# Performance work log

Hardware: AMD Instinct MI355X
Metric: run time of the kernel (lower is better)

Reference implementation:

```python
import jax, jax.numpy as jnp
import numpy as np

B, L, H, T = 32, 512, 1024, 67


def setup_inputs() -> dict:
    key = jax.random.key(0)
    ks = jax.random.split(key, 7)
    hidden = jax.random.normal(ks[0], (B, L, H), jnp.float32)
    labels = jax.random.randint(ks[1], (B, L), 0, T)
    # contiguous valid-length mask; torchcrf requires mask[:, 0] == True
    lengths = jax.random.randint(ks[2], (B,), L // 2, L + 1)
    mask = jnp.arange(L)[None, :] < lengths[:, None]  # bool [B, L]
    W = jax.random.normal(ks[3], (H, T), jnp.float32) / np.float32(np.sqrt(H))
    b = jnp.zeros((T,), jnp.float32)
    u = lambda k, s: jax.random.uniform(k, s, jnp.float32, -0.1, 0.1)  # torchcrf init
    return dict(hidden=hidden, W=W, b=b,
                start_transitions=u(ks[4], (T,)),
                end_transitions=u(ks[5], (T,)),
                transitions=u(ks[6], (T, T)),
                labels=labels, mask=mask)


def crf_log_likelihood(emissions, tags, mask, start, end, trans):
    # emissions [B,L,T], tags [B,L] int, mask [B,L] bool. Returns sum llh over batch.
    maskf = mask.astype(emissions.dtype)
    # --- numerator: score of gold path (fully vectorized) ---
    emit = jnp.take_along_axis(emissions, tags[..., None], axis=2)[..., 0]  # [B,L]
    tr = trans[tags[:, :-1], tags[:, 1:]]                                   # [B,L-1]
    seq_ends = mask.sum(1) - 1
    last_tags = jnp.take_along_axis(tags, seq_ends[:, None], axis=1)[:, 0]
    numerator = (start[tags[:, 0]] + (emit * maskf).sum(1)
                 + (tr * maskf[:, 1:]).sum(1) + end[last_tags])
    # --- denominator: log-partition via batched scan over time ---
    alpha0 = start[None, :] + emissions[:, 0]  # [B,T]
    def step(alpha, x):
        e_t, m_t = x  # [B,T], [B]
        nxt = jax.scipy.special.logsumexp(
            alpha[:, :, None] + trans[None, :, :] + e_t[:, None, :], axis=1)
        return jnp.where(m_t[:, None], nxt, alpha), None
    xs = (jnp.moveaxis(emissions[:, 1:], 1, 0), jnp.moveaxis(mask[:, 1:], 1, 0))
    alpha, _ = jax.lax.scan(step, alpha0, xs)
    denominator = jax.scipy.special.logsumexp(alpha + end[None, :], axis=1)
    return (numerator - denominator).sum()


def viterbi_decode(emissions, mask, start, end, trans):
    # Returns padded [B,L] int tags (padded positions set to 0).
    score0 = start[None, :] + emissions[:, 0]  # [B,T]
    def fstep(score, x):
        e_t, m_t = x
        bc = score[:, :, None] + trans[None, :, :]  # [B, prev T, cur T]
        idx = jnp.argmax(bc, axis=1)                # [B,T] best prev tag per cur
        best = jnp.max(bc, axis=1) + e_t
        return jnp.where(m_t[:, None], best, score), idx
    xs = (jnp.moveaxis(emissions[:, 1:], 1, 0), jnp.moveaxis(mask[:, 1:], 1, 0))
    score, hist = jax.lax.scan(fstep, score0, xs)   # hist [L-1,B,T]
    last = jnp.argmax(score + end[None, :], axis=1)  # [B] tag at last valid pos
    def bstep(cur, x):
        h_t, m_t = x
        out = cur  # tag at position t
        prev = jnp.take_along_axis(h_t, cur[:, None], axis=1)[:, 0]
        return jnp.where(m_t, prev, cur), out
    xs_rev = (hist[::-1], jnp.moveaxis(mask[:, 1:], 1, 0)[::-1])
    cur0, outs = jax.lax.scan(bstep, last, xs_rev)
    tags = jnp.concatenate([cur0[None, :], outs[::-1]], axis=0).T  # [B,L]
    return jnp.where(mask, tags, 0)


def reference(hidden, W, b, start_transitions, end_transitions, transitions, labels, mask):
    # dropout is identity in eval; leaky_relu negative_slope=0.01 matches torch default
    x = jax.nn.leaky_relu(hidden)
    token_scores = jax.nn.log_softmax(x @ W + b, axis=-1)  # [B,L,T]
    llh = crf_log_likelihood(token_scores, labels, mask,
                             start_transitions, end_transitions, transitions)
    loss = -llh / hidden.shape[0]
    tags = viterbi_decode(token_scores, mask,
                          start_transitions, end_transitions, transitions)
    return loss, tags
```

## Files before the change

kernel.cpp:

```cpp
#include <hip/hip_runtime.h>
#include <math.h>

constexpr int NB = 32;
constexpr int NL = 512;
constexpr int NH = 1024;
constexpr int NT = 67;

__device__ __forceinline__ float wave_max_f(float v) {
#pragma unroll
  for (int o = 32; o > 0; o >>= 1) v = fmaxf(v, __shfl_xor(v, o));
  return v;
}
__device__ __forceinline__ float wave_min_f(float v) {
#pragma unroll
  for (int o = 32; o > 0; o >>= 1) v = fminf(v, __shfl_xor(v, o));
  return v;
}
__device__ __forceinline__ float wave_sum_f(float v) {
#pragma unroll
  for (int o = 32; o > 0; o >>= 1) v += __shfl_xor(v, o);
  return v;
}
__device__ __forceinline__ int wave_sum_i(int v) {
#pragma unroll
  for (int o = 32; o > 0; o >>= 1) v += __shfl_xor(v, o);
  return v;
}

#define DPPF(OLDV, X, CTRL)                                                     \
  __int_as_float(__builtin_amdgcn_update_dpp(__float_as_int(OLDV),              \
                                             __float_as_int(X), (CTRL), 0xf,   \
                                             0xf, false))

__device__ __forceinline__ float wave_max_dpp(float x) {
  x = fmaxf(x, DPPF(x, x, 0x111));
  x = fmaxf(x, DPPF(x, x, 0x112));
  x = fmaxf(x, DPPF(x, x, 0x114));
  x = fmaxf(x, DPPF(x, x, 0x118));
  x = fmaxf(x, DPPF(x, x, 0x142));
  x = fmaxf(x, DPPF(x, x, 0x143));
  return __int_as_float(__builtin_amdgcn_readlane(__float_as_int(x), 63));
}
__device__ __forceinline__ float wave_sum_dpp(float x) {
  x += DPPF(0.f, x, 0x111);
  x += DPPF(0.f, x, 0x112);
  x += DPPF(0.f, x, 0x114);
  x += DPPF(0.f, x, 0x118);
  x += DPPF(0.f, x, 0x142);
  x += DPPF(0.f, x, 0x143);
  return __int_as_float(__builtin_amdgcn_readlane(__float_as_int(x), 63));
}

#define LGKM_BARRIER() asm volatile("s_waitcnt lgkmcnt(0)" ::: "memory")

__device__ __forceinline__ float rdlane(float v, int l) {
  return __int_as_float(__builtin_amdgcn_readlane(__float_as_int(v), l));
}
__device__ __forceinline__ float rdfirst(float v) {
  return __int_as_float(__builtin_amdgcn_readfirstlane(__float_as_int(v)));
}

constexpr int KR = 16, KC = 64;

__global__ __launch_bounds__(256) void k_scores(const float* __restrict__ hidden,
                                                const float* __restrict__ W,
                                                const float* __restrict__ bias,
                                                float* __restrict__ scores) {
  __shared__ float A[KR][KC + 1];
  __shared__ float Wg[KC * 96];
  __shared__ float Pm[KR][17];
  __shared__ float Ps[KR][17];
  __shared__ float Lse[KR];

  const int tid = threadIdx.x;
  const int r = tid & 15;
  const int cg = tid >> 4;
  const int c0 = cg * 5;
  const size_t r0 = (size_t)blockIdx.x * KR;

  float acc0 = 0.f, acc1 = 0.f, acc2 = 0.f, acc3 = 0.f, acc4 = 0.f;

  for (int kc = 0; kc < NH; kc += KC) {
    __syncthreads();
    {
      int row = tid >> 4, c4 = tid & 15;
      float4 v = *reinterpret_cast<const float4*>(&hidden[(r0 + row) * NH + kc + c4 * 4]);
      v.x = v.x > 0.f ? v.x : 0.01f * v.x;
      v.y = v.y > 0.f ? v.y : 0.01f * v.y;
      v.z = v.z > 0.f ? v.z : 0.01f * v.z;
      v.w = v.w > 0.f ? v.w : 0.01f * v.w;
      A[row][c4 * 4 + 0] = v.x;
      A[row][c4 * 4 + 1] = v.y;
      A[row][c4 * 4 + 2] = v.z;
      A[row][c4 * 4 + 3] = v.w;
    }
#pragma unroll
    for (int rep = 0; rep < 17; ++rep) {
      int idx = rep * 256 + tid;
      if (idx < KC * NT) {
        int k = idx / NT, t = idx - k * NT;
        int g = t / 5, m = t - g * 5;
        Wg[k * 96 + g * 6 + m] = W[(size_t)(kc + k) * NT + t];
      }
    }
    __syncthreads();
#pragma unroll 4
    for (int k = 0; k < KC; ++k) {
      float a = A[r][k];
      const float* wr = &Wg[k * 96 + cg * 6];
      float2 wa = *reinterpret_cast<const float2*>(wr);
      float2 wb = *reinterpret_cast<const float2*>(wr + 2);
      float w4 = wr[4];
      acc0 = fmaf(a, wa.x, acc0);
      acc1 = fmaf(a, wa.y, acc1);
      acc2 = fmaf(a, wb.x, acc2);
      acc3 = fmaf(a, wb.y, acc3);
      acc4 = fmaf(a, w4, acc4);
    }
  }
  __syncthreads();

  float acc[5] = {acc0, acc1, acc2, acc3, acc4};
  float pm = -INFINITY;
#pragma unroll
  for (int i = 0; i < 5; ++i) {
    int t = c0 + i;
    if (t < NT) {
      acc[i] += bias[t];
      pm = fmaxf(pm, acc[i]);
    }
  }
  Pm[r][cg] = pm;
  __syncthreads();
  float M = -INFINITY;
#pragma unroll
  for (int g = 0; g < 16; ++g) M = fmaxf(M, Pm[r][g]);
  float ps = 0.f;
#pragma unroll
  for (int i = 0; i < 5; ++i) {
    int t = c0 + i;
    if (t < NT) ps += expf(acc[i] - M);
  }
  Ps[r][cg] = ps;
  __syncthreads();
  if (cg == 0) {
    float s = 0.f;
#pragma unroll
    for (int g = 0; g < 16; ++g) s += Ps[r][g];
    Lse[r] = M + logf(s);
  }
  __syncthreads();
  float lse = Lse[r];
  float* Lb = &Wg[0];
#pragma unroll
  for (int i = 0; i < 5; ++i) {
    int t = c0 + i;
    if (t < NT) Lb[r * 68 + t] = acc[i] - lse;
  }
  __syncthreads();
#pragma unroll
  for (int rep = 0; rep < 5; ++rep) {
    int idx = rep * 256 + tid;
    if (idx < KR * NT) {
      int row = idx / NT, t = idx - row * NT;
      scores[(r0 + row) * NT + t] = Lb[row * 68 + t];
    }
  }
}

constexpr int VOF_TL = 0;
constexpr int VOF_H1 = 18496;
constexpr int VOF_GP = 35904;
constexpr int VOF_FJ = 53312;
constexpr int VOF_BJ = 53584;
constexpr int VOF_JP = 53856;
constexpr int VOF_JI = 54128;
constexpr int LDSV = 54144;

__global__ __launch_bounds__(128) void k_scan(const float* __restrict__ scores,
                                              const float* __restrict__ trans,
                                              const float* __restrict__ startv,
                                              const float* __restrict__ endv,
                                              const int* __restrict__ labels,
                                              const int* __restrict__ maskp,
                                              float* __restrict__ wsA,
                                              float* __restrict__ wsB,
                                              float* __restrict__ wsNum,
                                              float* __restrict__ tags_out) {
  extern __shared__ char smem[];
  const int lane = threadIdx.x & 63;
  const int wid = threadIdx.x >> 6;

  if (blockIdx.x < NB) {
    const int b = blockIdx.x;
    const float* sc = scores + (size_t)b * NL * NT;
    const int* mk = maskp + b * NL;

    if (wid == 0) {
      const int* lb = labels + b * NL;
      float* pb = (float*)(smem);

      float ET0[NT];
#pragma unroll
      for (int i = 0; i < NT; ++i) ET0[i] = __expf(trans[i * NT + lane]);
      float E3[3], E3b[3];
      const int r2 = (lane < 3) ? (64 + lane) : 66;
#pragma unroll
      for (int k = 0; k < 3; ++k) {
        E3[k] = __expf(trans[lane * NT + 64 + k]);
        E3b[k] = (lane < 3) ? __expf(trans[r2 * NT + 64 + k]) : 0.f;
      }
      float a0 = startv[lane] + sc[lane];
      float a1 = (lane < 3) ? (startv[64 + lane] + sc[64 + lane]) : 0.f;

      float e0 = sc[NT + lane];
      float e1 = (lane < 3) ? sc[NT + 64 + lane] : 0.f;
      for (int t = 1; t < 256; ++t) {
        float e0n = 0.f, e1n = 0.f;
        if (t < 255) {
          e0n = sc[(t + 1) * NT + lane];
          e1n = (lane < 3) ? sc[(t + 1) * NT + 64 + lane] : 0.f;
        }
        float M = rdfirst(a0);
        float q = __expf(a0 - M);
        float q2 = (lane < 3) ? __expf(a1 - M) : 0.f;
        pb[lane] = q;
        if (lane < 3) pb[64 + lane] = q2;
        LGKM_BARRIER();
        float s0 = 0, s1 = 0, s2 = 0, s3 = 0;
#pragma unroll
        for (int i4 = 0; i4 < 16; ++i4) {
          float4 pv = *reinterpret_cast<const float4*>(&pb[i4 * 4]);
          s0 = fmaf(pv.x, ET0[4 * i4 + 0], s0);
          s1 = fmaf(pv.y, ET0[4 * i4 + 1], s1);
          s2 = fmaf(pv.z, ET0[4 * i4 + 2], s2);
          s3 = fmaf(pv.w, ET0[4 * i4 + 3], s3);
        }
        {
          float p64 = pb[64], p65 = pb[65], p66 = pb[66];
          s0 = fmaf(p64, ET0[64], s0);
          s1 = fmaf(p65, ET0[65], s1);
          s2 = fmaf(p66, ET0[66], s2);
        }
        float S = (s0 + s1) + (s2 + s3);
        float x0 = wave_sum_dpp(fmaf(q, E3[0], q2 * E3b[0]));
        float x1 = wave_sum_dpp(fmaf(q, E3[1], q2 * E3b[1]));
        float x2 = wave_sum_dpp(fmaf(q, E3[2], q2 * E3b[2]));
        a0 = e0 + M + __logf(S);
        if (lane < 3) {
          float Sx = (lane == 0) ? x0 : ((lane == 1) ? x1 : x2);
          a1 = e1 + M + __logf(Sx);
        }
        e0 = e0n;
        e1 = e1n;
      }
      wsA[b * 68 + lane] = a0;
      if (lane < 3) wsA[b * 68 + 64 + lane] = a1;

      float esum = 0.f, trsum = 0.f;
      int lenc = 0;
#pragma unroll
      for (int rr = 0; rr < 8; ++rr) {
        int t = lane + 64 * rr;
        int m = mk[t];
        int lab = lb[t];
        if (m) {
          esum += sc[t * NT + lab];
          lenc += 1;
          if (t > 0) trsum += trans[lb[t - 1] * NT + lab];
        }
      }
      esum = wave_sum_f(esum);
      trsum = wave_sum_f(trsum);
      int len = wave_sum_i(lenc);
      if (lane == 0) wsNum[b] = startv[lb[0]] + esum + trsum + endv[lb[len - 1]];
    } else {
      float* pb = (float*)(smem + 512);

      float ER[NT];
#pragma unroll
      for (int j = 0; j < NT; ++j) ER[j] = __expf(trans[lane * NT + j]);
      float EC3[3], EC3b[3];
#pragma unroll
      for (int k = 0; k < 3; ++k) {
        EC3[k] = __expf(trans[(64 + k) * NT + lane]);
        EC3b[k] = (lane < 3) ? __expf(trans[(64 + k) * NT + 64 + lane]) : 0.f;
      }
      float b0 = endv[lane];
      float b1 = (lane < 3) ? endv[64 + lane] : 0.f;

      float e0 = sc[511 * NT + lane];
      float e1 = (lane < 3) ? sc[511 * NT + 64 + lane] : 0.f;
      int mt = mk[511];
      for (int t = 511; t >= 256; --t) {
        float e0n = 0.f, e1n = 0.f;
        int mtn = 0;
        if (t > 256) {
          e0n = sc[(t - 1) * NT + lane];
          e1n = (lane < 3) ? sc[(t - 1) * NT + 64 + lane] : 0.f;
          mtn = mk[t - 1];
        }
        float u = e0 + b0;
        float u2 = (lane < 3) ? (e1 + b1) : 0.f;
        float M = rdfirst(u);
        float q = __expf(u - M);
        float q2 = (lane < 3) ? __expf(u2 - M) : 0.f;
        pb[lane] = q;
        if (lane < 3) pb[64 + lane] = q2;
        LGKM_BARRIER();
        float s0 = 0, s1 = 0, s2 = 0, s3 = 0;
#pragma unroll
        for (int i4 = 0; i4 < 16; ++i4) {
          float4 pv = *reinterpret_cast<const float4*>(&pb[i4 * 4]);
          s0 = fmaf(pv.x, ER[4 * i4 + 0], s0);
          s1 = fmaf(pv.y, ER[4 * i4 + 1], s1);
          s2 = fmaf(pv.z, ER[4 * i4 + 2], s2);
          s3 = fmaf(pv.w, ER[4 * i4 + 3], s3);
        }
        {
          float p64 = pb[64], p65 = pb[65], p66 = pb[66];
          s0 = fmaf(p64, ER[64], s0);
          s1 = fmaf(p65, ER[65], s1);
          s2 = fmaf(p66, ER[66], s2);
        }
        float S = (s0 + s1) + (s2 + s3);
        float x0 = wave_sum_dpp(fmaf(q, EC3[0], q2 * EC3b[0]));
        float x1 = wave_sum_dpp(fmaf(q, EC3[1], q2 * EC3b[1]));
        float x2 = wave_sum_dpp(fmaf(q, EC3[2], q2 * EC3b[2]));
        if (mt) {
          b0 = M + __logf(S);
          if (lane < 3) {
            float Sx = (lane == 0) ? x0 : ((lane == 1) ? x1 : x2);
            b1 = M + __logf(Sx);
          }
        }
        e0 = e0n;
        e1 = e1n;
        mt = mtn;
      }
      wsB[b * 68 + lane] = b0;
      if (lane < 3) wsB[b * 68 + 64 + lane] = b1;
    }
  } else {
    const int b = blockIdx.x - NB;
    const float* sc = scores + (size_t)b * NL * NT;
    const int* mk = maskp + b * NL;
    float* out = tags_out + (size_t)b * NL;
    float* Tl = (float*)(smem + VOF_TL);
    unsigned char* h1f = (unsigned char*)(smem + VOF_H1);
    unsigned char* gp = (unsigned char*)(smem + VOF_GP);
    float* fj = (float*)(smem + VOF_FJ);
    float* bj = (float*)(smem + VOF_BJ);
    int* jp = (int*)(smem + VOF_JP);
    int* ji = (int*)(smem + VOF_JI);

    for (int idx = threadIdx.x; idx < NT * NT; idx += 128) {
      int i = idx / NT, j = idx - i * NT;
      Tl[i * 68 + j] = trans[idx];
    }
    for (int idx = threadIdx.x; idx < 68; idx += 128) {
      Tl[idx * 68 + 67] = 0.f;
      Tl[67 * 68 + idx] = 0.f;
    }
    __syncthreads();

    float lmin = 1e30f, lmax = -1e30f;
    for (int idx = lane; idx < NT * NT; idx += 64) {
      int i = idx / NT, j = idx - i * NT;
      float v = Tl[i * 68 + j];
      lmin = fminf(lmin, v);
      lmax = fmaxf(lmax, v);
    }
    const float trspan = wave_min_f(lmin) - wave_max_f(lmax) - 1e-5f;
    int lenc = 0;
#pragma unroll
    for (int rr = 0; rr < 8; ++rr) lenc += (mk[lane + 64 * rr] ? 1 : 0);
    const int len = wave_sum_i(lenc);

    if (wid == 0) {
      const int j2col = 64 + (lane & 3);
      float s0 = startv[lane] + sc[lane];
      float s1 = (lane < 3) ? (startv[64 + lane] + sc[64 + lane]) : -INFINITY;
      for (int t = 1; t < 256; ++t) {
        float e0 = sc[t * NT + lane];
        float e1 = (lane < 3) ? sc[t * NT + 64 + lane] : 0.f;
        float Smax = wave_max_dpp(fmaxf(s0, s1));
        float thr = Smax + trspan;
        unsigned long long cm = __ballot(s0 >= thr);
        unsigned em = (unsigned)__ballot((lane < 3) && (s1 >= thr)) & 7u;
        float m0 = -INFINITY, m1 = -INFINITY;
        int a0i = 0, a1i = 0;
        while (cm) {
          int c0 = (int)__builtin_ctzll(cm);
          unsigned long long n1 = cm & (cm - 1);
          int c1 = n1 ? (int)__builtin_ctzll(n1) : c0;
          unsigned long long n2 = n1 ? (n1 & (n1 - 1)) : 0;
          int c2 = n2 ? (int)__builtin_ctzll(n2) : c0;
          unsigned long long n3 = n2 ? (n2 & (n2 - 1)) : 0;
          int c3 = n3 ? (int)__builtin_ctzll(n3) : c0;
          cm = n3 ? (n3 & (n3 - 1)) : 0;
          float ta0 = Tl[c0 * 68 + lane], tb0 = Tl[c0 * 68 + j2col];
          float ta1 = Tl[c1 * 68 + lane], tb1 = Tl[c1 * 68 + j2col];
          float ta2 = Tl[c2 * 68 + lane], tb2 = Tl[c2 * 68 + j2col];
          float ta3 = Tl[c3 * 68 + lane], tb3 = Tl[c3 * 68 + j2col];
          float v0 = rdlane(s0, c0), v1 = rdlane(s0, c1);
          float v2 = rdlane(s0, c2), v3 = rdlane(s0, c3);
          float x;
          x = v0 + ta0; if (x > m0) { m0 = x; a0i = c0; }
          x = v1 + ta1; if (x > m0) { m0 = x; a0i = c1; }
          x = v2 + ta2; if (x > m0) { m0 = x; a0i = c2; }
          x = v3 + ta3; if (x > m0) { m0 = x; a0i = c3; }
          x = v0 + tb0; if (x > m1) { m1 = x; a1i = c0; }
          x = v1 + tb1; if (x > m1) { m1 = x; a1i = c1; }
          x = v2 + tb2; if (x > m1) { m1 = x; a1i = c2; }
          x = v3 + tb3; if (x > m1) { m1 = x; a1i = c3; }
        }
        while (em) {
          int eb = (int)__builtin_ctz(em);
          em &= em - 1;
          int c = 64 + eb;
          float scc = rdlane(s1, eb);
          float x0 = scc + Tl[c * 68 + lane];
          float x1 = scc + Tl[c * 68 + j2col];
          if (x0 > m0) { m0 = x0; a0i = c; }
          if (x1 > m1) { m1 = x1; a1i = c; }
        }
        h1f[t * 68 + lane] = (unsigned char)a0i;
        if (lane < 3) h1f[t * 68 + 64 + lane] = (unsigned char)a1i;
        s0 = m0 + e0;
        if (lane < 3) s1 = m1 + e1;
      }
      fj[lane] = s0;
      if (lane < 3) fj[64 + lane] = s1;
      __syncthreads();
      __syncthreads();
      int jstar = ji[0];
      for (int p = len + lane; p < NL; p += 64) out[p] = 0.f;
      if (lane == 0) {
        int cur = jstar;
        for (int p = 255; p >= 1; --p) {
          out[p] = (float)cur;
          cur = h1f[p * 68 + cur];
        }
        out[0] = (float)cur;
      }
    } else {
      const int i2 = 64 + (lane & 3);
      float b0 = 0.f, b1 = -INFINITY;
      if (len > 256) {
        b0 = sc[(size_t)(len - 1) * NT + lane] + endv[lane];
        b1 = (lane < 3) ? (sc[(size_t)(len - 1) * NT + 64 + lane] + endv[64 + lane])
                        : -INFINITY;
        for (int t = len - 2; t >= 256; --t) {
          float e0 = sc[t * NT + lane];
          float e1 = (lane < 3) ? sc[t * NT + 64 + lane] : 0.f;
          float Bmax = wave_max_dpp(fmaxf(b0, b1));
          float thr = Bmax + trspan;
          unsigned long long cm = __ballot(b0 >= thr);
          unsigned em = (unsigned)__ballot((lane < 3) && (b1 >= thr)) & 7u;
          float m0 = -INFINITY, m1 = -INFINITY;
          int a0i = 0, a1i = 0;
          while (cm) {
            int c0 = (int)__builtin_ctzll(cm);
            unsigned long long n1 = cm & (cm - 1);
            int c1 = n1 ? (int)__builtin_ctzll(n1) : c0;
            unsigned long long n2 = n1 ? (n1 & (n1 - 1)) : 0;
            int c2 = n2 ? (int)__builtin_ctzll(n2) : c0;
            unsigned long long n3 = n2 ? (n2 & (n2 - 1)) : 0;
            int c3 = n3 ? (int)__builtin_ctzll(n3) : c0;
            cm = n3 ? (n3 & (n3 - 1)) : 0;
            float ta0 = Tl[lane * 68 + c0], tb0 = Tl[i2 * 68 + c0];
            float ta1 = Tl[lane * 68 + c1], tb1 = Tl[i2 * 68 + c1];
            float ta2 = Tl[lane * 68 + c2], tb2 = Tl[i2 * 68 + c2];
            float ta3 = Tl[lane * 68 + c3], tb3 = Tl[i2 * 68 + c3];
            float v0 = rdlane(b0, c0), v1 = rdlane(b0, c1);
            float v2 = rdlane(b0, c2), v3 = rdlane(b0, c3);
            float x;
            x = v0 + ta0; if (x > m0) { m0 = x; a0i = c0; }
            x = v1 + ta1; if (x > m0) { m0 = x; a0i = c1; }
            x = v2 + ta2; if (x > m0) { m0 = x; a0i = c2; }
            x = v3 + ta3; if (x > m0) { m0 = x; a0i = c3; }
            x = v0 + tb0; if (x > m1) { m1 = x; a1i = c0; }
            x = v1 + tb1; if (x > m1) { m1 = x; a1i = c1; }
            x = v2 + tb2; if (x > m1) { m1 = x; a1i = c2; }
            x = v3 + tb3; if (x > m1) { m1 = x; a1i = c3; }
          }
          while (em) {
            int eb = (int)__builtin_ctz(em);
            em &= em - 1;
            int c = 64 + eb;
            float scc = rdlane(b1, eb);
            float x0 = scc + Tl[lane * 68 + c];
            float x1 = scc + Tl[i2 * 68 + c];
            if (x0 > m0) { m0 = x0; a0i = c; }
            if (x1 > m1) { m1 = x1; a1i = c; }
          }
          gp[(t + 1 - 256) * 68 + lane] = (unsigned char)a0i;
          if (lane < 3) gp[(t + 1 - 256) * 68 + 64 + lane] = (unsigned char)a1i;
          b0 = e0 + m0;
          if (lane < 3) b1 = e1 + m1;
        }
        bj[lane] = b0;
        if (lane < 3) bj[64 + lane] = b1;
      }
      __syncthreads();
      float ci, ci2;
      int jpi = 0, jpi2 = 0;
      if (len > 256) {
        ci = -INFINITY;
        ci2 = -INFINITY;
        for (int j = 0; j < NT; ++j) {
          float bv = bj[j];
          float x = Tl[lane * 68 + j] + bv;
          if (x > ci) { ci = x; jpi = j; }
          if (lane < 3) {
            float x2 = Tl[(64 + lane) * 68 + j] + bv;
            if (x2 > ci2) { ci2 = x2; jpi2 = j; }
          }
        }
      } else {
        ci = endv[lane];
        ci2 = (lane < 3) ? endv[64 + lane] : -INFINITY;
      }
      float v0 = fj[lane] + ci;
      float v1 = (lane < 3) ? (fj[64 + lane] + ci2) : -INFINITY;
      float bv_;
      int bi_;
      if (v1 > v0) { bv_ = v1; bi_ = 64 + lane; } else { bv_ = v0; bi_ = lane; }
#pragma unroll
      for (int o = 32; o > 0; o >>= 1) {
        float ov = __shfl_xor(bv_, o);
        int oi = __shfl_xor(bi_, o);
        if (ov > bv_ || (ov == bv_ && oi < bi_)) { bv_ = ov; bi_ = oi; }
      }
      jp[lane] = jpi;
      if (lane < 3) jp[64 + lane] = jpi2;
      LGKM_BARRIER();
      int s256 = (len > 256) ? jp[bi_] : 0;
      if (lane == 0) {
        ji[0] = bi_;
        ji[1] = s256;
      }
      __syncthreads();
      if (len > 256 && lane == 0) {
        int cur = ji[1];
        int p = 256;
        while (true) {
          out[p] = (float)cur;
          ++p;
          if (p >= len) break;
          cur = gp[(p - 256) * 68 + cur];
        }
      }
    }
  }
}

__global__ __launch_bounds__(256) void k_final(const float* __restrict__ wsA,
                                               const float* __restrict__ wsB,
                                               const float* __restrict__ wsNum,
                                               float* __restrict__ out) {
  const int tid = threadIdx.x;
  const int w = tid >> 6, lane = tid & 63;
  float acc = 0.f;
  for (int s = w; s < NB; s += 4) {
    float v = wsA[s * 68 + lane] + wsB[s * 68 + lane];
    float v2 = (lane < 3) ? (wsA[s * 68 + 64 + lane] + wsB[s * 68 + 64 + lane])
                          : -INFINITY;
    float M = wave_max_dpp(fmaxf(v, v2));
    float e = __expf(v - M) + ((lane < 3) ? __expf(v2 - M) : 0.f);
    float den = M + __logf(wave_sum_dpp(e));
    acc += wsNum[s] - den;
  }
  __shared__ float part[4];
  if (lane == 0) part[w] = acc;
  __syncthreads();
  if (tid == 0) out[0] = -(part[0] + part[1] + part[2] + part[3]) / (float)NB;
}

extern "C" void kernel_launch(void* const* d_in, const int* in_sizes, int n_in,
                              void* d_out, int out_size, void* d_ws, size_t ws_size,
                              hipStream_t stream) {
  const float* hidden = (const float*)d_in[0];
  const float* W = (const float*)d_in[1];
  const float* bias = (const float*)d_in[2];
  const float* startv = (const float*)d_in[3];
  const float* endv = (const float*)d_in[4];
  const float* trans = (const float*)d_in[5];
  const int* labels = (const int*)d_in[6];
  const int* maskp = (const int*)d_in[7];
  float* out = (float*)d_out;

  float* scores = (float*)d_ws;
  float* wsA = scores + (size_t)NB * NL * NT;
  float* wsB = wsA + NB * 68;
  float* wsNum = wsB + NB * 68;

  hipLaunchKernelGGL(k_scores, dim3((NB * NL) / KR), dim3(256), 0, stream,
                     hidden, W, bias, scores);
  hipLaunchKernelGGL(k_scan, dim3(2 * NB), dim3(128), LDSV, stream,
                     scores, trans, startv, endv, labels, maskp,
                     wsA, wsB, wsNum, out + 1);
  hipLaunchKernelGGL(k_final, dim3(1), dim3(256), 0, stream,
                     wsA, wsB, wsNum, out);
}
```

Measured before the change: 385.1 us.

## Rewrite score GEMM tiling and switch CRF scans to scaled linear-domain recurrences

The projection kernel now gives each block 64 rows. Each wave owns 17 tag columns, hidden is transposed into double-buffered LDS with register prefetch, and W is read straight from global memory. The forward/backward CRF scans move from log-space to probability space: the LDS broadcast is replaced by readlane dot products, and rescaling happens only every 8 steps, so most per-step exp/log and LDS round-trips go away. The Viterbi paths add two-step emission prefetch and a transposed transition table. They also compose backpointers into 64-step checkpoint maps so backtracking runs in parallel across 4 lanes instead of serially. The price is more LDS, more shuffles per step, and a numerical-range risk from less frequent rescaling.

```diff
diff --git a/kernel.cpp b/kernel.cpp
--- a/kernel.cpp
+++ b/kernel.cpp
@@ -56,126 +56,139 @@
 __device__ __forceinline__ float rdlane(float v, int l) {
   return __int_as_float(__builtin_amdgcn_readlane(__float_as_int(v), l));
 }
-__device__ __forceinline__ float rdfirst(float v) {
-  return __int_as_float(__builtin_amdgcn_readfirstlane(__float_as_int(v)));
-}
-
-constexpr int KR = 16, KC = 64;
+
+#define BCAST_DOT(RES, PV, PV2, ETARR)                                         \
+  {                                                                            \
+    float _s0 = 0.f, _s1 = 0.f, _s2 = 0.f, _s3 = 0.f;                          \
+    _Pragma("unroll") for (int _i = 0; _i < 64; _i += 4) {                     \
+      _s0 = fmaf(rdlane(PV, _i + 0), ETARR[_i + 0], _s0);                      \
+      _s1 = fmaf(rdlane(PV, _i + 1), ETARR[_i + 1], _s1);                      \
+      _s2 = fmaf(rdlane(PV, _i + 2), ETARR[_i + 2], _s2);                      \
+      _s3 = fmaf(rdlane(PV, _i + 3), ETARR[_i + 3], _s3);                      \
+    }                                                                          \
+    _s0 = fmaf(rdlane(PV2, 0), ETARR[64], _s0);                                \
+    _s1 = fmaf(rdlane(PV2, 1), ETARR[65], _s1);                                \
+    _s2 = fmaf(rdlane(PV2, 2), ETARR[66], _s2);                                \
+    RES = (_s0 + _s1) + (_s2 + _s3);                                           \
+  }
+
+constexpr int SKC = 128;
 
 __global__ __launch_bounds__(256) void k_scores(const float* __restrict__ hidden,
                                                 const float* __restrict__ W,
                                                 const float* __restrict__ bias,
                                                 float* __restrict__ scores) {
-  __shared__ float A[KR][KC + 1];
-  __shared__ float Wg[KC * 96];
-  __shared__ float Pm[KR][17];
-  __shared__ float Ps[KR][17];
-  __shared__ float Lse[KR];
+  __shared__ float AT[2][SKC][65];
+  __shared__ float Pm[4][64];
+  __shared__ float Ps[4][64];
 
   const int tid = threadIdx.x;
-  const int r = tid & 15;
-  const int cg = tid >> 4;
-  const int c0 = cg * 5;
-  const size_t r0 = (size_t)blockIdx.x * KR;
-
-  float acc0 = 0.f, acc1 = 0.f, acc2 = 0.f, acc3 = 0.f, acc4 = 0.f;
-
-  for (int kc = 0; kc < NH; kc += KC) {
-    __syncthreads();
-    {
-      int row = tid >> 4, c4 = tid & 15;
-      float4 v = *reinterpret_cast<const float4*>(&hidden[(r0 + row) * NH + kc + c4 * 4]);
-      v.x = v.x > 0.f ? v.x : 0.01f * v.x;
-      v.y = v.y > 0.f ? v.y : 0.01f * v.y;
-      v.z = v.z > 0.f ? v.z : 0.01f * v.z;
-      v.w = v.w > 0.f ? v.w : 0.01f * v.w;
-      A[row][c4 * 4 + 0] = v.x;
-      A[row][c4 * 4 + 1] = v.y;
-      A[row][c4 * 4 + 2] = v.z;
-      A[row][c4 * 4 + 3] = v.w;
-    }
-#pragma unroll
-    for (int rep = 0; rep < 17; ++rep) {
-      int idx = rep * 256 + tid;
-      if (idx < KC * NT) {
-        int k = idx / NT, t = idx - k * NT;
-        int g = t / 5, m = t - g * 5;
-        Wg[k * 96 + g * 6 + m] = W[(size_t)(kc + k) * NT + t];
-      }
-    }
-    __syncthreads();
-#pragma unroll 4
-    for (int k = 0; k < KC; ++k) {
-      float a = A[r][k];
-      const float* wr = &Wg[k * 96 + cg * 6];
-      float2 wa = *reinterpret_cast<const float2*>(wr);
-      float2 wb = *reinterpret_cast<const float2*>(wr + 2);
-      float w4 = wr[4];
-      acc0 = fmaf(a, wa.x, acc0);
-      acc1 = fmaf(a, wa.y, acc1);
-      acc2 = fmaf(a, wb.x, acc2);
-      acc3 = fmaf(a, wb.y, acc3);
-      acc4 = fmaf(a, w4, acc4);
-    }
+  const int lane = tid & 63;
+  const int wv = __builtin_amdgcn_readfirstlane(tid >> 6);
+  const size_t r0 = (size_t)blockIdx.x * 64;
+
+  const int cb = (wv == 3) ? 50 : wv * 17;
+  const int rstart = (wv == 3) ? 1 : 0;
+  const float* __restrict__ Wu = W + cb;
+
+  float acc[17];
+#pragma unroll
+  for (int i = 0; i < 17; ++i) acc[i] = 0.f;
+
+  float4 st[8];
+#pragma unroll
+  for (int it = 0; it < 8; ++it) {
+    int flat = it * 256 + tid;
+    int row = flat >> 5, k4 = flat & 31;
+    st[it] = *reinterpret_cast<const float4*>(&hidden[(r0 + row) * NH + k4 * 4]);
+  }
+#pragma unroll
+  for (int it = 0; it < 8; ++it) {
+    int flat = it * 256 + tid;
+    int row = flat >> 5, k4 = flat & 31;
+    float4 v = st[it];
+    v.x = fmaxf(v.x, 0.01f * v.x);
+    v.y = fmaxf(v.y, 0.01f * v.y);
+    v.z = fmaxf(v.z, 0.01f * v.z);
+    v.w = fmaxf(v.w, 0.01f * v.w);
+    AT[0][k4 * 4 + 0][row] = v.x;
+    AT[0][k4 * 4 + 1][row] = v.y;
+    AT[0][k4 * 4 + 2][row] = v.z;
+    AT[0][k4 * 4 + 3][row] = v.w;
   }
   __syncthreads();
 
-  float acc[5] = {acc0, acc1, acc2, acc3, acc4};
+  for (int ch = 0; ch < 8; ++ch) {
+    const int buf = ch & 1;
+    if (ch < 7) {
+      const int kn = (ch + 1) * SKC;
+#pragma unroll
+      for (int it = 0; it < 8; ++it) {
+        int flat = it * 256 + tid;
+        int row = flat >> 5, k4 = flat & 31;
+        st[it] = *reinterpret_cast<const float4*>(&hidden[(r0 + row) * NH + kn + k4 * 4]);
+      }
+    }
+    const float* wrow = Wu + (size_t)ch * SKC * NT;
+#pragma unroll 2
+    for (int k = 0; k < SKC; ++k) {
+      float a = AT[buf][k][lane];
+      const float* wr = wrow + k * NT;
+#pragma unroll
+      for (int c = 0; c < 17; ++c) acc[c] = fmaf(a, wr[c], acc[c]);
+    }
+    if (ch < 7) {
+#pragma unroll
+      for (int it = 0; it < 8; ++it) {
+        int flat = it * 256 + tid;
+        int row = flat >> 5, k4 = flat & 31;
+        float4 v = st[it];
+        v.x = fmaxf(v.x, 0.01f * v.x);
+        v.y = fmaxf(v.y, 0.01f * v.y);
+        v.z = fmaxf(v.z, 0.01f * v.z);
+        v.w = fmaxf(v.w, 0.01f * v.w);
+        AT[buf ^ 1][k4 * 4 + 0][row] = v.x;
+        AT[buf ^ 1][k4 * 4 + 1][row] = v.y;
+        AT[buf ^ 1][k4 * 4 + 2][row] = v.z;
+        AT[buf ^ 1][k4 * 4 + 3][row] = v.w;
+      }
+    }
+    __syncthreads();
+  }
+
+#pragma unroll
+  for (int c = 0; c < 17; ++c) acc[c] += bias[cb + c];
   float pm = -INFINITY;
 #pragma unroll
-  for (int i = 0; i < 5; ++i) {
-    int t = c0 + i;
-    if (t < NT) {
-      acc[i] += bias[t];
-      pm = fmaxf(pm, acc[i]);
-    }
-  }
-  Pm[r][cg] = pm;
+  for (int c = 0; c < 17; ++c)
+    if (c >= rstart) pm = fmaxf(pm, acc[c]);
+  Pm[wv][lane] = pm;
   __syncthreads();
-  float M = -INFINITY;
-#pragma unroll
-  for (int g = 0; g < 16; ++g) M = fmaxf(M, Pm[r][g]);
+  float M = fmaxf(fmaxf(Pm[0][lane], Pm[1][lane]), fmaxf(Pm[2][lane], Pm[3][lane]));
   float ps = 0.f;
 #pragma unroll
-  for (int i = 0; i < 5; ++i) {
-    int t = c0 + i;
-    if (t < NT) ps += expf(acc[i] - M);
-  }
-  Ps[r][cg] = ps;
+  for (int c = 0; c < 17; ++c)
+    if (c >= rstart) ps += expf(acc[c] - M);
+  Ps[wv][lane] = ps;
   __syncthreads();
-  if (cg == 0) {
-    float s = 0.f;
-#pragma unroll
-    for (int g = 0; g < 16; ++g) s += Ps[r][g];
-    Lse[r] = M + logf(s);
-  }
-  __syncthreads();
-  float lse = Lse[r];
-  float* Lb = &Wg[0];
-#pragma unroll
-  for (int i = 0; i < 5; ++i) {
-    int t = c0 + i;
-    if (t < NT) Lb[r * 68 + t] = acc[i] - lse;
-  }
-  __syncthreads();
-#pragma unroll
-  for (int rep = 0; rep < 5; ++rep) {
-    int idx = rep * 256 + tid;
-    if (idx < KR * NT) {
-      int row = idx / NT, t = idx - row * NT;
-      scores[(r0 + row) * NT + t] = Lb[row * 68 + t];
-    }
-  }
+  float S = ((Ps[0][lane] + Ps[1][lane]) + (Ps[2][lane] + Ps[3][lane]));
+  float lse = M + logf(S);
+#pragma unroll
+  for (int c = 0; c < 17; ++c)
+    if (c >= rstart) scores[(r0 + lane) * NT + cb + c] = acc[c] - lse;
 }
 
 constexpr int VOF_TL = 0;
-constexpr int VOF_H1 = 18496;
-constexpr int VOF_GP = 35904;
-constexpr int VOF_FJ = 53312;
-constexpr int VOF_BJ = 53584;
-constexpr int VOF_JP = 53856;
-constexpr int VOF_JI = 54128;
-constexpr int LDSV = 54144;
+constexpr int VOF_TT = 18496;
+constexpr int VOF_H1 = 36992;
+constexpr int VOF_GP = 54400;
+constexpr int VOF_FJ = 71808;
+constexpr int VOF_BJ = 72080;
+constexpr int VOF_JP = 72352;
+constexpr int VOF_CKF = 72624;
+constexpr int VOF_CKB = 72896;
+constexpr int VOF_JI = 73104;
+constexpr int LDSV = 73120;
 
 __global__ __launch_bounds__(128) void k_scan(const float* __restrict__ scores,
                                               const float* __restrict__ trans,
@@ -198,8 +211,6 @@
 
     if (wid == 0) {
       const int* lb = labels + b * NL;
-      float* pb = (float*)(smem);
-
       float ET0[NT];
 #pragma unroll
       for (int i = 0; i < NT; ++i) ET0[i] = __expf(trans[i * NT + lane]);
@@ -210,52 +221,39 @@
         E3[k] = __expf(trans[lane * NT + 64 + k]);
         E3b[k] = (lane < 3) ? __expf(trans[r2 * NT + 64 + k]) : 0.f;
       }
-      float a0 = startv[lane] + sc[lane];
-      float a1 = (lane < 3) ? (startv[64 + lane] + sc[64 + lane]) : 0.f;
-
-      float e0 = sc[NT + lane];
-      float e1 = (lane < 3) ? sc[NT + 64 + lane] : 0.f;
+      float P = __expf(startv[lane] + sc[lane]);
+      float P2 = (lane < 3) ? __expf(startv[64 + lane] + sc[64 + lane]) : 0.f;
+      float logsc = 0.f;
+      float eA0 = sc[NT + lane];
+      float eA1 = (lane < 3) ? sc[NT + 64 + lane] : 0.f;
+      float eB0 = sc[2 * NT + lane];
+      float eB1 = (lane < 3) ? sc[2 * NT + 64 + lane] : 0.f;
       for (int t = 1; t < 256; ++t) {
-        float e0n = 0.f, e1n = 0.f;
-        if (t < 255) {
-          e0n = sc[(t + 1) * NT + lane];
-          e1n = (lane < 3) ? sc[(t + 1) * NT + 64 + lane] : 0.f;
-        }
-        float M = rdfirst(a0);
-        float q = __expf(a0 - M);
-        float q2 = (lane < 3) ? __expf(a1 - M) : 0.f;
-        pb[lane] = q;
-        if (lane < 3) pb[64 + lane] = q2;
-        LGKM_BARRIER();
-        float s0 = 0, s1 = 0, s2 = 0, s3 = 0;
-#pragma unroll
-        for (int i4 = 0; i4 < 16; ++i4) {
-          float4 pv = *reinterpret_cast<const float4*>(&pb[i4 * 4]);
-          s0 = fmaf(pv.x, ET0[4 * i4 + 0], s0);
-          s1 = fmaf(pv.y, ET0[4 * i4 + 1], s1);
-          s2 = fmaf(pv.z, ET0[4 * i4 + 2], s2);
-          s3 = fmaf(pv.w, ET0[4 * i4 + 3], s3);
-        }
-        {
-          float p64 = pb[64], p65 = pb[65], p66 = pb[66];
-          s0 = fmaf(p64, ET0[64], s0);
-          s1 = fmaf(p65, ET0[65], s1);
-          s2 = fmaf(p66, ET0[66], s2);
-        }
-        float S = (s0 + s1) + (s2 + s3);
-        float x0 = wave_sum_dpp(fmaf(q, E3[0], q2 * E3b[0]));
-        float x1 = wave_sum_dpp(fmaf(q, E3[1], q2 * E3b[1]));
-        float x2 = wave_sum_dpp(fmaf(q, E3[2], q2 * E3b[2]));
-        a0 = e0 + M + __logf(S);
-        if (lane < 3) {
-          float Sx = (lane == 0) ? x0 : ((lane == 1) ? x1 : x2);
-          a1 = e1 + M + __logf(Sx);
-        }
-        e0 = e0n;
-        e1 = e1n;
-      }
-      wsA[b * 68 + lane] = a0;
-      if (lane < 3) wsA[b * 68 + 64 + lane] = a1;
+        float pe = __expf(eA0);
+        float pe2 = (lane < 3) ? __expf(eA1) : 0.f;
+        eA0 = eB0;
+        eA1 = eB1;
+        if (t < 254) {
+          eB0 = sc[(t + 2) * NT + lane];
+          eB1 = (lane < 3) ? sc[(t + 2) * NT + 64 + lane] : 0.f;
+        }
+        float S;
+        BCAST_DOT(S, P, P2, ET0);
+        float x0 = wave_sum_dpp(fmaf(P, E3[0], P2 * E3b[0]));
+        float x1 = wave_sum_dpp(fmaf(P, E3[1], P2 * E3b[1]));
+        float x2 = wave_sum_dpp(fmaf(P, E3[2], P2 * E3b[2]));
+        P = pe * S;
+        if (lane < 3) P2 = pe2 * ((lane == 0) ? x0 : ((lane == 1) ? x1 : x2));
+        if ((t & 7) == 0) {
+          float m = wave_max_dpp(fmaxf(P, P2));
+          float inv = 1.0f / m;
+          P *= inv;
+          P2 *= inv;
+          logsc += __logf(m);
+        }
+      }
+      wsA[b * 68 + lane] = logsc + __logf(P);
+      if (lane < 3) wsA[b * 68 + 64 + lane] = logsc + __logf(P2);
 
       float esum = 0.f, trsum = 0.f;
       int lenc = 0;
@@ -275,8 +273,6 @@
       int len = wave_sum_i(lenc);
       if (lane == 0) wsNum[b] = startv[lb[0]] + esum + trsum + endv[lb[len - 1]];
     } else {
-      float* pb = (float*)(smem + 512);
-
       float ER[NT];
 #pragma unroll
       for (int j = 0; j < NT; ++j) ER[j] = __expf(trans[lane * NT + j]);
@@ -286,60 +282,48 @@
         EC3[k] = __expf(trans[(64 + k) * NT + lane]);
         EC3b[k] = (lane < 3) ? __expf(trans[(64 + k) * NT + 64 + lane]) : 0.f;
       }
-      float b0 = endv[lane];
-      float b1 = (lane < 3) ? endv[64 + lane] : 0.f;
-
-      float e0 = sc[511 * NT + lane];
-      float e1 = (lane < 3) ? sc[511 * NT + 64 + lane] : 0.f;
-      int mt = mk[511];
+      float Q = __expf(endv[lane]);
+      float Q2 = (lane < 3) ? __expf(endv[64 + lane]) : 0.f;
+      float logsc = 0.f;
+      float eA0 = sc[511 * NT + lane];
+      float eA1 = (lane < 3) ? sc[511 * NT + 64 + lane] : 0.f;
+      int mA = mk[511];
+      float eB0 = sc[510 * NT + lane];
+      float eB1 = (lane < 3) ? sc[510 * NT + 64 + lane] : 0.f;
+      int mB = mk[510];
       for (int t = 511; t >= 256; --t) {
-        float e0n = 0.f, e1n = 0.f;
-        int mtn = 0;
-        if (t > 256) {
-          e0n = sc[(t - 1) * NT + lane];
-          e1n = (lane < 3) ? sc[(t - 1) * NT + 64 + lane] : 0.f;
-          mtn = mk[t - 1];
-        }
-        float u = e0 + b0;
-        float u2 = (lane < 3) ? (e1 + b1) : 0.f;
-        float M = rdfirst(u);
-        float q = __expf(u - M);
-        float q2 = (lane < 3) ? __expf(u2 - M) : 0.f;
-        pb[lane] = q;
-        if (lane < 3) pb[64 + lane] = q2;
-        LGKM_BARRIER();
-        float s0 = 0, s1 = 0, s2 = 0, s3 = 0;
-#pragma unroll
-        for (int i4 = 0; i4 < 16; ++i4) {
-          float4 pv = *reinterpret_cast<const float4*>(&pb[i4 * 4]);
-          s0 = fmaf(pv.x, ER[4 * i4 + 0], s0);
-          s1 = fmaf(pv.y, ER[4 * i4 + 1], s1);
-          s2 = fmaf(pv.z, ER[4 * i4 + 2], s2);
-          s3 = fmaf(pv.w, ER[4 * i4 + 3], s3);
-        }
-        {
-          float p64 = pb[64], p65 = pb[65], p66 = pb[66];
-          s0 = fmaf(p64, ER[64], s0);
-          s1 = fmaf(p65, ER[65], s1);
-          s2 = fmaf(p66, ER[66], s2);
-        }
-        float S = (s0 + s1) + (s2 + s3);
-        float x0 = wave_sum_dpp(fmaf(q, EC3[0], q2 * EC3b[0]));
-        float x1 = wave_sum_dpp(fmaf(q, EC3[1], q2 * EC3b[1]));
-        float x2 = wave_sum_dpp(fmaf(q, EC3[2], q2 * EC3b[2]));
+        float ue0 = __expf(eA0);
+        float ue1 = (lane < 3) ? __expf(eA1) : 0.f;
+        int mt = mA;
+        eA0 = eB0;
+        eA1 = eB1;
+        mA = mB;
+        if (t > 257) {
+          eB0 = sc[(t - 2) * NT + lane];
+          eB1 = (lane < 3) ? sc[(t - 2) * NT + 64 + lane] : 0.f;
+          mB = mk[t - 2];
+        }
+        float u = ue0 * Q;
+        float u2 = ue1 * Q2;
+        float S;
+        BCAST_DOT(S, u, u2, ER);
+        float x0 = wave_sum_dpp(fmaf(u, EC3[0], u2 * EC3b[0]));
+        float x1 = wave_sum_dpp(fmaf(u, EC3[1], u2 * EC3b[1]));
+        float x2 = wave_sum_dpp(fmaf(u, EC3[2], u2 * EC3b[2]));
         if (mt) {
-          b0 = M + __logf(S);
-          if (lane < 3) {
-            float Sx = (lane == 0) ? x0 : ((lane == 1) ? x1 : x2);
-            b1 = M + __logf(Sx);
-          }
-        }
-        e0 = e0n;
-        e1 = e1n;
-        mt = mtn;
-      }
-      wsB[b * 68 + lane] = b0;
-      if (lane < 3) wsB[b * 68 + 64 + lane] = b1;
+          Q = S;
+          if (lane < 3) Q2 = (lane == 0) ? x0 : ((lane == 1) ? x1 : x2);
+        }
+        if ((t & 7) == 0) {
+          float m = wave_max_dpp(fmaxf(Q, Q2));
+          float inv = 1.0f / m;
+          Q *= inv;
+          Q2 *= inv;
+          logsc += __logf(m);
+        }
+      }
+      wsB[b * 68 + lane] = logsc + __logf(Q);
+      if (lane < 3) wsB[b * 68 + 64 + lane] = logsc + __logf(Q2);
     }
   } else {
     const int b = blockIdx.x - NB;
@@ -347,20 +331,27 @@
     const int* mk = maskp + b * NL;
     float* out = tags_out + (size_t)b * NL;
     float* Tl = (float*)(smem + VOF_TL);
+    float* TlT = (float*)(smem + VOF_TT);
     unsigned char* h1f = (unsigned char*)(smem + VOF_H1);
     unsigned char* gp = (unsigned char*)(smem + VOF_GP);
     float* fj = (float*)(smem + VOF_FJ);
     float* bj = (float*)(smem + VOF_BJ);
     int* jp = (int*)(smem + VOF_JP);
+    unsigned char* ckF = (unsigned char*)(smem + VOF_CKF);
+    unsigned char* ckB = (unsigned char*)(smem + VOF_CKB);
     int* ji = (int*)(smem + VOF_JI);
 
     for (int idx = threadIdx.x; idx < NT * NT; idx += 128) {
       int i = idx / NT, j = idx - i * NT;
-      Tl[i * 68 + j] = trans[idx];
+      float v = trans[idx];
+      Tl[i * 68 + j] = v;
+      TlT[j * 68 + i] = v;
     }
     for (int idx = threadIdx.x; idx < 68; idx += 128) {
       Tl[idx * 68 + 67] = 0.f;
       Tl[67 * 68 + idx] = 0.f;
+      TlT[idx * 68 + 67] = 0.f;
+      TlT[67 * 68 + idx] = 0.f;
     }
     __syncthreads();
 
@@ -381,9 +372,19 @@
       const int j2col = 64 + (lane & 3);
       float s0 = startv[lane] + sc[lane];
       float s1 = (lane < 3) ? (startv[64 + lane] + sc[64 + lane]) : -INFINITY;
+      int cmp = lane, cmp2 = 64 + lane;
+      float eA0 = sc[NT + lane];
+      float eA1 = (lane < 3) ? sc[NT + 64 + lane] : 0.f;
+      float eB0 = sc[2 * NT + lane];
+      float eB1 = (lane < 3) ? sc[2 * NT + 64 + lane] : 0.f;
       for (int t = 1; t < 256; ++t) {
-        float e0 = sc[t * NT + lane];
-        float e1 = (lane < 3) ? sc[t * NT + 64 + lane] : 0.f;
+        float e0 = eA0, e1 = eA1;
+        eA0 = eB0;
+        eA1 = eB1;
+        if (t < 254) {
+          eB0 = sc[(t + 2) * NT + lane];
+          eB1 = (lane < 3) ? sc[(t + 2) * NT + 64 + lane] : 0.f;
+        }
         float Smax = wave_max_dpp(fmaxf(s0, s1));
         float thr = Smax + trspan;
         unsigned long long cm = __ballot(s0 >= thr);
@@ -427,6 +428,21 @@
         }
         h1f[t * 68 + lane] = (unsigned char)a0i;
         if (lane < 3) h1f[t * 68 + 64 + lane] = (unsigned char)a1i;
+        int gA = __shfl(cmp, a0i & 63);
+        int gB = __shfl(cmp2, (a0i >= 64) ? (a0i - 64) : 0);
+        int nc = (a0i < 64) ? gA : gB;
+        int gA2 = __shfl(cmp, a1i & 63);
+        int gB2 = __shfl(cmp2, (a1i >= 64) ? (a1i - 64) : 0);
+        int nc2 = (a1i < 64) ? gA2 : gB2;
+        cmp = nc;
+        cmp2 = nc2;
+        if ((t & 63) == 0) {
+          int slot = t >> 6;
+          ckF[slot * 68 + lane] = (unsigned char)cmp;
+          if (lane < 3) ckF[slot * 68 + 64 + lane] = (unsigned char)cmp2;
+          cmp = lane;
+          cmp2 = 64 + lane;
+        }
         s0 = m0 + e0;
         if (lane < 3) s1 = m1 + e1;
       }
@@ -436,24 +452,44 @@
       __syncthreads();
       int jstar = ji[0];
       for (int p = len + lane; p < NL; p += 64) out[p] = 0.f;
-      if (lane == 0) {
-        int cur = jstar;
-        for (int p = 255; p >= 1; --p) {
+      int gA = __shfl(cmp, jstar & 63);
+      int gB = __shfl(cmp2, (jstar >= 64) ? (jstar - 64) : 0);
+      int s192 = (jstar < 64) ? gA : gB;
+      int s128 = ckF[3 * 68 + s192];
+      int s64 = ckF[2 * 68 + s128];
+      if (lane < 4) {
+        int cur;
+        if (lane == 3) cur = jstar;
+        else if (lane == 2) cur = h1f[192 * 68 + s192];
+        else if (lane == 1) cur = h1f[128 * 68 + s128];
+        else cur = h1f[64 * 68 + s64];
+        int base = lane * 64;
+        for (int s = 0; s < 64; ++s) {
+          int p = base + 63 - s;
           out[p] = (float)cur;
-          cur = h1f[p * 68 + cur];
-        }
-        out[0] = (float)cur;
+          if (p > 0) cur = h1f[p * 68 + cur];
+        }
       }
     } else {
       const int i2 = 64 + (lane & 3);
+      int cmpB = lane, cmpB2 = 64 + lane;
       float b0 = 0.f, b1 = -INFINITY;
       if (len > 256) {
         b0 = sc[(size_t)(len - 1) * NT + lane] + endv[lane];
         b1 = (lane < 3) ? (sc[(size_t)(len - 1) * NT + 64 + lane] + endv[64 + lane])
                         : -INFINITY;
+        float eA0 = sc[(size_t)(len - 2) * NT + lane];
+        float eA1 = (lane < 3) ? sc[(size_t)(len - 2) * NT + 64 + lane] : 0.f;
+        float eB0 = sc[(size_t)(len - 3) * NT + lane];
+        float eB1 = (lane < 3) ? sc[(size_t)(len - 3) * NT + 64 + lane] : 0.f;
         for (int t = len - 2; t >= 256; --t) {
-          float e0 = sc[t * NT + lane];
-          float e1 = (lane < 3) ? sc[t * NT + 64 + lane] : 0.f;
+          float e0 = eA0, e1 = eA1;
+          eA0 = eB0;
+          eA1 = eB1;
+          if (t > 257) {
+            eB0 = sc[(t - 2) * NT + lane];
+            eB1 = (lane < 3) ? sc[(t - 2) * NT + 64 + lane] : 0.f;
+          }
           float Bmax = wave_max_dpp(fmaxf(b0, b1));
           float thr = Bmax + trspan;
           unsigned long long cm = __ballot(b0 >= thr);
@@ -469,10 +505,10 @@
             unsigned long long n3 = n2 ? (n2 & (n2 - 1)) : 0;
             int c3 = n3 ? (int)__builtin_ctzll(n3) : c0;
             cm = n3 ? (n3 & (n3 - 1)) : 0;
-            float ta0 = Tl[lane * 68 + c0], tb0 = Tl[i2 * 68 + c0];
-            float ta1 = Tl[lane * 68 + c1], tb1 = Tl[i2 * 68 + c1];
-            float ta2 = Tl[lane * 68 + c2], tb2 = Tl[i2 * 68 + c2];
-            float ta3 = Tl[lane * 68 + c3], tb3 = Tl[i2 * 68 + c3];
+            float ta0 = TlT[c0 * 68 + lane], tb0 = TlT[c0 * 68 + i2];
+            float ta1 = TlT[c1 * 68 + lane], tb1 = TlT[c1 * 68 + i2];
+            float ta2 = TlT[c2 * 68 + lane], tb2 = TlT[c2 * 68 + i2];
+            float ta3 = TlT[c3 * 68 + lane], tb3 = TlT[c3 * 68 + i2];
             float v0 = rdlane(b0, c0), v1 = rdlane(b0, c1);
             float v2 = rdlane(b0, c2), v3 = rdlane(b0, c3);
             float x;
@@ -490,13 +526,28 @@
             em &= em - 1;
             int c = 64 + eb;
             float scc = rdlane(b1, eb);
-            float x0 = scc + Tl[lane * 68 + c];
-            float x1 = scc + Tl[i2 * 68 + c];
+            float x0 = scc + TlT[c * 68 + lane];
+            float x1 = scc + TlT[c * 68 + i2];
             if (x0 > m0) { m0 = x0; a0i = c; }
             if (x1 > m1) { m1 = x1; a1i = c; }
           }
           gp[(t + 1 - 256) * 68 + lane] = (unsigned char)a0i;
           if (lane < 3) gp[(t + 1 - 256) * 68 + 64 + lane] = (unsigned char)a1i;
+          int gA = __shfl(cmpB, a0i & 63);
+          int gB = __shfl(cmpB2, (a0i >= 64) ? (a0i - 64) : 0);
+          int nc = (a0i < 64) ? gA : gB;
+          int gA2 = __shfl(cmpB, a1i & 63);
+          int gB2 = __shfl(cmpB2, (a1i >= 64) ? (a1i - 64) : 0);
+          int nc2 = (a1i < 64) ? gA2 : gB2;
+          cmpB = nc;
+          cmpB2 = nc2;
+          if (t == 448 || t == 384 || t == 320) {
+            int slot = (t - 320) >> 6;
+            ckB[slot * 68 + lane] = (unsigned char)cmpB;
+            if (lane < 3) ckB[slot * 68 + 64 + lane] = (unsigned char)cmpB2;
+            cmpB = lane;
+            cmpB2 = 64 + lane;
+          }
           b0 = e0 + m0;
           if (lane < 3) b1 = e1 + m1;
         }
@@ -511,10 +562,10 @@
         ci2 = -INFINITY;
         for (int j = 0; j < NT; ++j) {
           float bv = bj[j];
-          float x = Tl[lane * 68 + j] + bv;
+          float x = TlT[j * 68 + lane] + bv;
           if (x > ci) { ci = x; jpi = j; }
           if (lane < 3) {
-            float x2 = Tl[(64 + lane) * 68 + j] + bv;
+            float x2 = TlT[j * 68 + 64 + lane] + bv;
             if (x2 > ci2) { ci2 = x2; jpi2 = j; }
           }
         }
@@ -542,14 +593,25 @@
         ji[1] = s256;
       }
       __syncthreads();
-      if (len > 256 && lane == 0) {
-        int cur = ji[1];
-        int p = 256;
-        while (true) {
-          out[p] = (float)cur;
-          ++p;
-          if (p >= len) break;
-          cur = gp[(p - 256) * 68 + cur];
+      if (len > 256) {
+        int s320 = 0, s384 = 0, s448 = 0;
+        if (len > 320) {
+          int gA = __shfl(cmpB, s256 & 63);
+          int gB = __shfl(cmpB2, (s256 >= 64) ? (s256 - 64) : 0);
+          s320 = (s256 < 64) ? gA : gB;
+        }
+        if (len > 384) s384 = ckB[0 * 68 + s320];
+        if (len > 448) s448 = ckB[1 * 68 + s384];
+        if (lane < 4) {
+          int t_c = 256 + lane * 64;
+          if (t_c < len) {
+            int cur = (lane == 0) ? s256 : (lane == 1) ? s320 : (lane == 2) ? s384 : s448;
+            int stop = min(t_c + 64, len);
+            for (int p = t_c; p < stop; ++p) {
+              out[p] = (float)cur;
+              cur = gp[(p + 1 - 256) * 68 + cur];
+            }
+          }
         }
       }
     }
@@ -596,7 +658,7 @@
   float* wsB = wsA + NB * 68;
   float* wsNum = wsB + NB * 68;
 
-  hipLaunchKernelGGL(k_scores, dim3((NB * NL) / KR), dim3(256), 0, stream,
+  hipLaunchKernelGGL(k_scores, dim3((NB * NL) / 64), dim3(256), 0, stream,
                      hidden, W, bias, scores);
   hipLaunchKernelGGL(k_scan, dim3(2 * NB), dim3(128), LDSV, stream,
                      scores, trans, startv, endv, labels, maskp,
```

Measured after the change: 432.6 us. 1.12x slower.
